# Kernel tuning notes

Hardware: AMD Instinct MI355X
Metric: run time of the kernel (lower is better)

Reference implementation:

```python
import jax, jax.numpy as jnp
import numpy as np

N_P = 50000   # number of 'place' nodes
N_A = 50000   # number of 'a_transition' nodes
E = 1600000   # edges per edge type
IN = 128      # input feature dim
OUT = 64      # HANConv out_channels
H = 4         # heads
D = OUT // H  # per-head dim
HID = 64      # decoder hidden
NEG_SLOPE = 0.2  # HANConv leaky_relu slope


def setup_inputs() -> dict:
    key = jax.random.key(0)
    ks = jax.random.split(key, 24)
    def nrm(i, shape, scale=1.0):
        return jax.random.normal(ks[i], shape, dtype=jnp.float32) * scale
    w = lambda i, shape, fan: nrm(i, shape, (1.0 / fan) ** 0.5)
    return {
        "x_place": nrm(0, (N_P, IN)),
        "x_atrans": nrm(1, (N_A, IN)),
        "e_pa_src": jax.random.randint(ks[2], (E,), 0, N_P),
        "e_pa_dst": jax.random.randint(ks[3], (E,), 0, N_A),
        "e_aa_src": jax.random.randint(ks[4], (E,), 0, N_A),
        "e_aa_dst": jax.random.randint(ks[5], (E,), 0, N_A),
        "e_ap_src": jax.random.randint(ks[6], (E,), 0, N_A),
        "e_ap_dst": jax.random.randint(ks[7], (E,), 0, N_P),
        "Wp_place": w(8, (IN, OUT), IN),
        "bp_place": jnp.zeros((OUT,), jnp.float32),
        "Wp_atrans": w(9, (IN, OUT), IN),
        "bp_atrans": jnp.zeros((OUT,), jnp.float32),
        "asrc_pa": w(10, (H, D), D),
        "adst_pa": w(11, (H, D), D),
        "asrc_aa": w(12, (H, D), D),
        "adst_aa": w(13, (H, D), D),
        "asrc_ap": w(14, (H, D), D),
        "adst_ap": w(15, (H, D), D),
        "Wk": w(16, (OUT, OUT), OUT),
        "bk": jnp.zeros((OUT,), jnp.float32),
        "q": w(17, (OUT,), OUT),
        "Wd1": w(18, (OUT, HID), OUT),
        "bd1": jnp.zeros((HID,), jnp.float32),
        "Wd2": w(19, (HID, 1), HID),
        "bd2": jnp.zeros((1,), jnp.float32),
    }


def _edge_conv(h_src, h_dst, a_src, a_dst, src, dst, n_dst):
    """HANConv node-level attention for one edge type.
    h_src: [N_src, H, D], h_dst: [N_dst, H, D]; returns relu-aggregated [n_dst, H*D]."""
    alpha = (h_src * a_src).sum(-1)[src] + (h_dst * a_dst).sum(-1)[dst]  # [E, H]
    alpha = jax.nn.leaky_relu(alpha, NEG_SLOPE)
    amax = jax.ops.segment_max(alpha, dst, num_segments=n_dst)
    amax = jnp.where(jnp.isfinite(amax), amax, 0.0)  # guard empty neighborhoods
    ex = jnp.exp(alpha - amax[dst])
    den = jax.ops.segment_sum(ex, dst, num_segments=n_dst) + 1e-16  # PyG softmax eps
    wgt = ex / den[dst]                           # scatter-softmax per dst node [E, H]
    msg = h_src[src] * wgt[:, :, None]            # [E, H, D]
    out = jax.ops.segment_sum(msg, dst, num_segments=n_dst)
    return jax.nn.relu(out.reshape(n_dst, H * D))


def _semantic(outs, q, Wk, bk):
    """HANConv semantic-level attention over edge-type embeddings."""
    stk = jnp.stack(outs)                                       # [T, N, OUT]
    score = (q * jnp.tanh(stk @ Wk + bk).mean(axis=1)).sum(-1)  # [T]
    attn = jax.nn.softmax(score)
    return jnp.einsum('t,tnc->nc', attn, stk)


def reference(x_place, x_atrans, e_pa_src, e_pa_dst, e_aa_src, e_aa_dst, e_ap_src, e_ap_dst,
              Wp_place, bp_place, Wp_atrans, bp_atrans,
              asrc_pa, adst_pa, asrc_aa, adst_aa, asrc_ap, adst_ap,
              Wk, bk, q, Wd1, bd1, Wd2, bd2):
    # per-node-type projection, split into heads
    h_p = (x_place @ Wp_place + bp_place).reshape(N_P, H, D)
    h_a = (x_atrans @ Wp_atrans + bp_atrans).reshape(N_A, H, D)
    # node-level attention per edge type
    out_pa = _edge_conv(h_p, h_a, asrc_pa, adst_pa, e_pa_src, e_pa_dst, N_A)
    out_aa = _edge_conv(h_a, h_a, asrc_aa, adst_aa, e_aa_src, e_aa_dst, N_A)
    out_ap = _edge_conv(h_a, h_p, asrc_ap, adst_ap, e_ap_src, e_ap_dst, N_P)
    # semantic-level attention per destination node type
    x_a = _semantic([out_pa, out_aa], q, Wk, bk)   # 'a_transition'
    _xp = _semantic([out_ap], q, Wk, bk)           # 'place' (computed by encoder, unused downstream)
    # decoder MLP on 'a_transition' + softmax over nodes (dim=0)
    z = jax.nn.relu(x_a @ Wd1 + bd1) @ Wd2 + bd2   # [N_A, 1]
    return jax.nn.softmax(z, axis=0)
```

## Files before the change

kernel.cpp:

```cpp
#include <hip/hip_runtime.h>
#include <hip/hip_fp16.h>
#include <math.h>

#define NP 50000
#define NA 50000
#define NE 1600000
#define IN_DIM 128
#define OUT_DIM 64

#define NB 391
#define BCAP 4608
#define P1_CHUNK 4096
#define P1_GRID ((NE + P1_CHUNK - 1) / P1_CHUNK)
#define PROJ_BLOCKS ((NP + 63) / 64)

typedef _Float16 v8h __attribute__((ext_vector_type(8)));
typedef _Float16 h2f __attribute__((ext_vector_type(2)));
typedef float    v4f __attribute__((ext_vector_type(4)));

__device__ inline float fast_tanh(float x) {
    const float e = __expf(2.f * x);
    return 1.f - 2.f / (e + 1.f);
}

__device__ inline float lane_f32(float v, int k) {
    return __builtin_bit_cast(float,
        __builtin_amdgcn_readlane(__builtin_bit_cast(int, v), k));
}

__global__ __launch_bounds__(256) void front_kernel(
    const float* __restrict__ xA, const float* __restrict__ WA, const float* __restrict__ bA,
    const float* __restrict__ xB, const float* __restrict__ WB, const float* __restrict__ bB,
    const float* __restrict__ a_pa_src, const float* __restrict__ a_pa_dst,
    const float* __restrict__ a_aa_src, const float* __restrict__ a_aa_dst,
    ushort* __restrict__ hA, ushort* __restrict__ hB,
    float* __restrict__ s_p_src_pa, float* __restrict__ s_a_dst_pa,
    float* __restrict__ s_a_src_aa, float* __restrict__ s_a_dst_aa,
    const int* __restrict__ srcA, const int* __restrict__ dstA,
    const int* __restrict__ srcB, const int* __restrict__ dstB,
    int* __restrict__ gpart, int* __restrict__ gcur)
{
    __shared__ __align__(16) char smem[22656];
    const int type = blockIdx.y;
    const int tid = threadIdx.x;

    if (blockIdx.x < P1_GRID) {
        const int* src = type ? srcB : srcA;
        const int* dst = type ? dstB : dstA;
        const int ebase = blockIdx.x * P1_CHUNK;
        const int ecount = min(P1_CHUNK, NE - ebase);

        int* hist   = (int*)smem;
        int* starts = hist + NB;
        int* offs2  = starts + NB;
        int* gbase  = offs2 + NB;
        unsigned* sorted = (unsigned*)(gbase + NB);

        for (int i = tid; i < NB; i += 256) hist[i] = 0;
        __syncthreads();
        for (int i = tid; i < ecount; i += 256)
            atomicAdd(&hist[dst[ebase + i] >> 7], 1);
        __syncthreads();
        if (tid < 64) {
            int carry = 0;
            for (int r = 0; r < 7; ++r) {
                const int idx = r * 64 + tid;
                const int v = (idx < NB) ? hist[idx] : 0;
                int s = v;
                #pragma unroll
                for (int off = 1; off < 64; off <<= 1) {
                    const int t = __shfl_up(s, off);
                    if (tid >= off) s += t;
                }
                if (idx < NB) { starts[idx] = carry + s - v; offs2[idx] = carry + s - v; }
                carry += __shfl(s, 63);
            }
        }
        __syncthreads();
        for (int i = tid; i < ecount; i += 256) {
            const int d = dst[ebase + i];
            const int s = src[ebase + i];
            const int bin = d >> 7;
            const int pos = atomicAdd(&offs2[bin], 1);
            sorted[pos] = ((unsigned)bin << 23) | ((unsigned)(d & 127) << 16) | (unsigned)s;
        }
        __syncthreads();
        for (int b = tid; b < NB; b += 256) {
            const int cnt = hist[b];
            const int flatb = type * NB + b;
            gbase[b] = cnt ? (flatb * BCAP + atomicAdd(&gcur[flatb], cnt)) : 0;
        }
        __syncthreads();
        for (int i = tid; i < ecount; i += 256) {
            const unsigned e = sorted[i];
            const int bin = e >> 23;
            gpart[gbase[bin] + (i - starts[bin])] = (int)(e & 0x7FFFFF);
        }
        return;
    }

    const int pbid = blockIdx.x - P1_GRID;
    const float* x = type ? xB : xA;
    const float* W = type ? WB : WA;
    const float* bias = type ? bB : bA;
    ushort* h_out  = type ? hB : hA;
    const float* c0 = type ? a_pa_dst : a_pa_src;
    float*       s0 = type ? s_a_dst_pa : s_p_src_pa;
    const float* c1 = type ? a_aa_src : nullptr;
    float*       s1 = type ? s_a_src_aa : nullptr;
    const float* c2 = type ? a_aa_dst : nullptr;
    float*       s2 = type ? s_a_dst_aa : nullptr;

    _Float16 (*Wt)[136] = (_Float16(*)[136])smem;
    {
        const float4* W4 = (const float4*)W;
        #pragma unroll
        for (int i = 0; i < 8; ++i) {
            const int f4i = tid + 256 * i;
            const float4 w = W4[f4i];
            const int k = f4i >> 4, c4 = (f4i & 15) * 4;
            Wt[c4 + 0][k] = (_Float16)w.x;
            Wt[c4 + 1][k] = (_Float16)w.y;
            Wt[c4 + 2][k] = (_Float16)w.z;
            Wt[c4 + 3][k] = (_Float16)w.w;
        }
    }
    __syncthreads();

    const int lane = tid & 63;
    const int wid = tid >> 6;
    const int node0 = (pbid * 4 + wid) * 16;
    if (node0 >= NP) return;
    const int m = lane & 15;
    const int quad = lane >> 4;

    v4f acc[4] = {};
    #pragma unroll
    for (int kc = 0; kc < 4; ++kc) {
        const int k0 = kc * 32 + quad * 8;
        const float4 xa = *(const float4*)(x + (size_t)(node0 + m) * IN_DIM + k0);
        const float4 xb2 = *(const float4*)(x + (size_t)(node0 + m) * IN_DIM + k0 + 4);
        v8h af;
        af[0] = (_Float16)xa.x;  af[1] = (_Float16)xa.y;
        af[2] = (_Float16)xa.z;  af[3] = (_Float16)xa.w;
        af[4] = (_Float16)xb2.x; af[5] = (_Float16)xb2.y;
        af[6] = (_Float16)xb2.z; af[7] = (_Float16)xb2.w;
        #pragma unroll
        for (int cb = 0; cb < 4; ++cb) {
            const v8h bf = *(const v8h*)&Wt[cb * 16 + m][k0];
            acc[cb] = __builtin_amdgcn_mfma_f32_16x16x32_f16(af, bf, acc[cb], 0, 0, 0);
        }
    }

    #pragma unroll
    for (int cb = 0; cb < 4; ++cb) {
        const int c = cb * 16 + m;
        const float bv = bias[c];
        float hv[4];
        #pragma unroll
        for (int r = 0; r < 4; ++r) {
            hv[r] = acc[cb][r] + bv;
            const int node = node0 + quad * 4 + r;
            h_out[(size_t)node * 64 + c] = __half_as_ushort(__float2half_rn(hv[r]));
        }
        #define DO_SCORE(A, S)                                         \
            if (A) {                                                   \
                const float av = (A)[c];                               \
                float v0 = hv[0]*av, v1 = hv[1]*av, v2 = hv[2]*av, v3 = hv[3]*av; \
                for (int msk = 1; msk <= 8; msk <<= 1) {               \
                    v0 += __shfl_xor(v0, msk);                         \
                    v1 += __shfl_xor(v1, msk);                         \
                    v2 += __shfl_xor(v2, msk);                         \
                    v3 += __shfl_xor(v3, msk);                         \
                }                                                      \
                if (m == 0) {                                          \
                    const int nb = node0 + quad * 4;                   \
                    (S)[(nb + 0) * 4 + cb] = v0;                       \
                    (S)[(nb + 1) * 4 + cb] = v1;                       \
                    (S)[(nb + 2) * 4 + cb] = v2;                       \
                    (S)[(nb + 3) * 4 + cb] = v3;                       \
                }                                                      \
            }
        DO_SCORE(c0, s0)
        DO_SCORE(c1, s1)
        DO_SCORE(c2, s2)
        #undef DO_SCORE
    }
}

__global__ __launch_bounds__(256) void bucket_sort_kernel(
    int* __restrict__ gpart, const int* __restrict__ gcur,
    int* __restrict__ recA, int* __restrict__ offsA,
    int* __restrict__ recB, int* __restrict__ offsB)
{
    const int b = blockIdx.x, type = blockIdx.y;
    int* rec  = type ? recB  : recA;
    int* offs = type ? offsB : offsA;
    const int flat = type * NB + b;
    const int region = flat * BCAP;
    const int cnt = gcur[flat];
    const int tid = threadIdx.x;

    __shared__ int hist[128];
    __shared__ int starts[128];
    __shared__ int offs2[128];
    __shared__ int red[4];
    __shared__ int sorted[BCAP];

    int p = 0;
    for (int i = tid; i < b; i += 256) p += gcur[type * NB + i];
    #pragma unroll
    for (int msk = 1; msk <= 32; msk <<= 1) p += __shfl_xor(p, msk);
    if ((tid & 63) == 0) red[tid >> 6] = p;
    if (tid < 128) hist[tid] = 0;
    __syncthreads();
    const int bst = red[0] + red[1] + red[2] + red[3];

    for (int i = tid; i < cnt; i += 256)
        atomicAdd(&hist[gpart[region + i] >> 16], 1);
    __syncthreads();
    if (tid < 64) {
        int carry = 0;
        for (int r = 0; r < 2; ++r) {
            const int idx = r * 64 + tid;
            const int v = hist[idx];
            int s = v;
            #pragma unroll
            for (int off = 1; off < 64; off <<= 1) {
                const int t = __shfl_up(s, off);
                if (tid >= off) s += t;
            }
            starts[idx] = carry + s - v;
            offs2[idx]  = carry + s - v;
            carry += __shfl(s, 63);
        }
    }
    __syncthreads();
    for (int i = tid; i < cnt; i += 256) {
        const int pk = gpart[region + i];
        const int pos = atomicAdd(&offs2[pk >> 16], 1);
        sorted[pos] = pk & 0xFFFF;
    }
    __syncthreads();
    for (int i = tid; i < cnt; i += 256) rec[bst + i] = sorted[i];
    if (tid < 128) {
        const int n = b * 128 + tid;
        if (n < NA) offs[n] = bst + starts[tid];
    }
    if (b == NB - 1 && tid == 0) offs[NA] = bst + cnt;
}

__global__ __launch_bounds__(256) void gather_kernel(
    const int* __restrict__ offsA, const int* __restrict__ recA,
    const ushort* __restrict__ hA, const float* __restrict__ ssA,
    const float* __restrict__ sdA, float* __restrict__ outA,
    const int* __restrict__ offsB, const int* __restrict__ recB,
    const ushort* __restrict__ hB, const float* __restrict__ ssB,
    const float* __restrict__ sdB, float* __restrict__ outB, int n_dst)
{
    const int type = blockIdx.y;
    const int* offs = type ? offsB : offsA;
    const int* rec  = type ? recB  : recA;
    const ushort* h_src = type ? hB : hA;
    const float* s_src = type ? ssB : ssA;
    const float* s_dst = type ? sdB : sdA;
    float* outbuf = type ? outB : outA;

    const int lane = threadIdx.x & 63;
    const int d = blockIdx.x * 4 + (threadIdx.x >> 6);
    if (d >= n_dst) return;
    const int q = lane & 7;
    const int sub = lane >> 3;
    const int h = q >> 1;
    const float sd = s_dst[d * 4 + h];
    const ushort* hq = h_src + (q << 3);
    const float* ss = s_src + h;
    const int beg = offs[d], end = offs[d + 1];

    float acc[8] = {};
    float wacc = 0.f;
    for (int base = beg; base < end; base += 64) {
        const int c64 = min(64, end - base);
        const int sv = (lane < c64) ? rec[base + lane] : 0;
        const int iters = (c64 + 7) >> 3;
        for (int it = 0; it < iters; ++it) {
            const int idx = it * 8 + sub;
            const int s = __shfl(sv, idx);
            if (idx < c64) {
                float alpha = ss[(size_t)s * 4] + sd;
                alpha = fmaxf(alpha, 0.2f * alpha);
                const float w = __expf(alpha);
                const uint4 pk = *(const uint4*)(hq + ((size_t)s << 6));
                const h2f a0 = __builtin_bit_cast(h2f, pk.x);
                const h2f a1 = __builtin_bit_cast(h2f, pk.y);
                const h2f a2 = __builtin_bit_cast(h2f, pk.z);
                const h2f a3 = __builtin_bit_cast(h2f, pk.w);
                acc[0] = fmaf((float)a0[0], w, acc[0]);
                acc[1] = fmaf((float)a0[1], w, acc[1]);
                acc[2] = fmaf((float)a1[0], w, acc[2]);
                acc[3] = fmaf((float)a1[1], w, acc[3]);
                acc[4] = fmaf((float)a2[0], w, acc[4]);
                acc[5] = fmaf((float)a2[1], w, acc[5]);
                acc[6] = fmaf((float)a3[0], w, acc[6]);
                acc[7] = fmaf((float)a3[1], w, acc[7]);
                wacc += w;
            }
        }
    }
    #pragma unroll
    for (int m = 8; m <= 32; m <<= 1) {
        #pragma unroll
        for (int j = 0; j < 8; ++j) acc[j] += __shfl_xor(acc[j], m);
        wacc += __shfl_xor(wacc, m);
    }
    if (sub == 0) {
        const float inv = 1.f / (wacc + 1e-16f);
        float4 o0, o1;
        o0.x = fmaxf(acc[0] * inv, 0.f);
        o0.y = fmaxf(acc[1] * inv, 0.f);
        o0.z = fmaxf(acc[2] * inv, 0.f);
        o0.w = fmaxf(acc[3] * inv, 0.f);
        o1.x = fmaxf(acc[4] * inv, 0.f);
        o1.y = fmaxf(acc[5] * inv, 0.f);
        o1.z = fmaxf(acc[6] * inv, 0.f);
        o1.w = fmaxf(acc[7] * inv, 0.f);
        float* op = outbuf + (size_t)d * 64 + q * 8;
        *(float4*)op = o0;
        *(float4*)(op + 4) = o1;
    }
}

#define SEM_BLOCKS 512
__global__ __launch_bounds__(256) void semantic_kernel(
    const float* __restrict__ out0, const float* __restrict__ out1,
    const float* __restrict__ Wk, const float* __restrict__ bk,
    float* __restrict__ sem, int n)
{
    const int c = threadIdx.x, ty = threadIdx.y;
    float wk[64];
    #pragma unroll
    for (int k = 0; k < 64; ++k) wk[k] = Wk[k * 64 + c];
    const float bkc = bk[c];
    float acc0 = 0.f, acc1 = 0.f;
    for (int node = blockIdx.x * 4 + ty; node < n; node += SEM_BLOCKS * 4) {
        const float n0 = out0[(size_t)node * 64 + c];
        const float n1 = out1[(size_t)node * 64 + c];
        float a0 = bkc, a1 = bkc;
        #pragma unroll
        for (int k = 0; k < 64; ++k) {
            a0 = fmaf(lane_f32(n0, k), wk[k], a0);
            a1 = fmaf(lane_f32(n1, k), wk[k], a1);
        }
        acc0 += fast_tanh(a0);
        acc1 += fast_tanh(a1);
    }
    __shared__ float red[2][4][64];
    red[0][ty][c] = acc0; red[1][ty][c] = acc1;
    __syncthreads();
    if (ty == 0) {
        atomicAdd(&sem[c],      red[0][0][c] + red[0][1][c] + red[0][2][c] + red[0][3][c]);
        atomicAdd(&sem[64 + c], red[1][0][c] + red[1][1][c] + red[1][2][c] + red[1][3][c]);
    }
}

__global__ __launch_bounds__(256) void decoder_kernel(
    const float* __restrict__ out0, const float* __restrict__ out1,
    const float* __restrict__ sem, const float* __restrict__ qv,
    const float* __restrict__ Wd1, const float* __restrict__ bd1,
    const float* __restrict__ Wd2, const float* __restrict__ bd2,
    float* __restrict__ z, int n)
{
    __shared__ float attn_s[2];
    const int c = threadIdx.x, ty = threadIdx.y;
    const int node = blockIdx.x * 4 + ty;

    if (ty == 0) {
        float v0 = sem[c] * qv[c];
        float v1 = sem[64 + c] * qv[c];
        for (int off = 32; off >= 1; off >>= 1) {
            v0 += __shfl_xor(v0, off);
            v1 += __shfl_xor(v1, off);
        }
        if (c == 0) {
            const float t0 = v0 / (float)NA, t1 = v1 / (float)NA;
            const float m = fmaxf(t0, t1);
            const float e0 = __expf(t0 - m), e1 = __expf(t1 - m);
            const float inv = 1.f / (e0 + e1);
            attn_s[0] = e0 * inv;
            attn_s[1] = e1 * inv;
        }
    }
    float wd[64];
    #pragma unroll
    for (int k = 0; k < 64; ++k) wd[k] = Wd1[k * 64 + c];
    __syncthreads();
    if (node >= n) return;
    const float a0 = attn_s[0], a1 = attn_s[1];
    const float xv = a0 * out0[(size_t)node * 64 + c]
                   + a1 * out1[(size_t)node * 64 + c];
    float acc = bd1[c];
    #pragma unroll
    for (int k = 0; k < 64; ++k)
        acc = fmaf(lane_f32(xv, k), wd[k], acc);
    float hv = fmaxf(acc, 0.f) * Wd2[c];
    for (int off = 32; off >= 1; off >>= 1) hv += __shfl_xor(hv, off);
    if (c == 0) z[node] = hv + bd2[0];
}

__global__ __launch_bounds__(256) void softmax_exp_kernel(
    const float* __restrict__ z, float* __restrict__ e,
    float* __restrict__ esum, int n)
{
    float part = 0.f;
    for (int i = blockIdx.x * 256 + threadIdx.x; i < n; i += gridDim.x * 256) {
        const float v = __expf(z[i]);
        e[i] = v;
        part += v;
    }
    for (int off = 32; off >= 1; off >>= 1) part += __shfl_xor(part, off);
    __shared__ float red[4];
    if ((threadIdx.x & 63) == 0) red[threadIdx.x >> 6] = part;
    __syncthreads();
    if (threadIdx.x == 0)
        atomicAdd(esum, red[0] + red[1] + red[2] + red[3]);
}

__global__ __launch_bounds__(256) void softmax_final_kernel(
    const float* __restrict__ e, const float* __restrict__ esum,
    float* __restrict__ out, int n)
{
    const int i = blockIdx.x * 256 + threadIdx.x;
    if (i < n) out[i] = e[i] / (*esum);
}

extern "C" void kernel_launch(void* const* d_in, const int* in_sizes, int n_in,
                              void* d_out, int out_size, void* d_ws, size_t ws_size,
                              hipStream_t stream)
{
    const float* x_place  = (const float*)d_in[0];
    const float* x_atrans = (const float*)d_in[1];
    const int* e_pa_src = (const int*)d_in[2];
    const int* e_pa_dst = (const int*)d_in[3];
    const int* e_aa_src = (const int*)d_in[4];
    const int* e_aa_dst = (const int*)d_in[5];
    const float* Wp_place  = (const float*)d_in[8];
    const float* bp_place  = (const float*)d_in[9];
    const float* Wp_atrans = (const float*)d_in[10];
    const float* bp_atrans = (const float*)d_in[11];
    const float* asrc_pa = (const float*)d_in[12];
    const float* adst_pa = (const float*)d_in[13];
    const float* asrc_aa = (const float*)d_in[14];
    const float* adst_aa = (const float*)d_in[15];
    const float* Wk  = (const float*)d_in[18];
    const float* bk  = (const float*)d_in[19];
    const float* q   = (const float*)d_in[20];
    const float* Wd1 = (const float*)d_in[21];
    const float* bd1 = (const float*)d_in[22];
    const float* Wd2 = (const float*)d_in[23];
    const float* bd2 = (const float*)d_in[24];
    float* out = (float*)d_out;

    float* ws = (float*)d_ws;
    size_t off = 0;
    auto alloc = [&](size_t n) {
        float* p = ws + off; off += (n + 3) & ~(size_t)3; return p;
    };

    ushort* h_p       = (ushort*)alloc((size_t)NP * 32);
    ushort* h_a       = (ushort*)alloc((size_t)NA * 32);
    float* s_p_src_pa = alloc((size_t)NP * 4);
    float* s_a_dst_pa = alloc((size_t)NA * 4);
    float* s_a_src_aa = alloc((size_t)NA * 4);
    float* s_a_dst_aa = alloc((size_t)NA * 4);
    float* out_pa     = alloc((size_t)NA * 64);
    float* out_aa     = alloc((size_t)NA * 64);
    int*   offs_pa    = (int*)alloc(NA + 1);
    int*   offs_aa    = (int*)alloc(NA + 1);
    int*   rec_pa     = (int*)alloc(NE);
    int*   rec_aa     = (int*)alloc(NE);
    int*   gcur       = (int*)alloc(2 * NB);
    float* sem        = alloc(128);
    float* esum       = alloc(4);
    float* zbuf       = alloc(NA);
    float* ebuf       = alloc(NA);
    int* gpart = (int*)out_pa;
    (void)ws_size; (void)in_sizes; (void)n_in; (void)out_size;

    const size_t zbytes = (size_t)((char*)(esum + 4) - (char*)gcur);
    hipMemsetAsync(gcur, 0, zbytes, stream);

    front_kernel<<<dim3(P1_GRID + PROJ_BLOCKS, 2), 256, 0, stream>>>(
        x_place, Wp_place, bp_place,
        x_atrans, Wp_atrans, bp_atrans,
        asrc_pa, adst_pa, asrc_aa, adst_aa,
        h_p, h_a,
        s_p_src_pa, s_a_dst_pa, s_a_src_aa, s_a_dst_aa,
        e_pa_src, e_pa_dst, e_aa_src, e_aa_dst, gpart, gcur);

    bucket_sort_kernel<<<dim3(NB, 2), 256, 0, stream>>>(
        gpart, gcur, rec_pa, offs_pa, rec_aa, offs_aa);

    gather_kernel<<<dim3((NA + 3) / 4, 2), 256, 0, stream>>>(
        offs_pa, rec_pa, h_p, s_p_src_pa, s_a_dst_pa, out_pa,
        offs_aa, rec_aa, h_a, s_a_src_aa, s_a_dst_aa, out_aa, NA);

    dim3 b64x4(64, 4);
    semantic_kernel<<<SEM_BLOCKS, b64x4, 0, stream>>>(out_pa, out_aa, Wk, bk, sem, NA);
    decoder_kernel<<<NA / 4, b64x4, 0, stream>>>(
        out_pa, out_aa, sem, q, Wd1, bd1, Wd2, bd2, zbuf, NA);
    softmax_exp_kernel<<<196, 256, 0, stream>>>(zbuf, ebuf, esum, NA);
    softmax_final_kernel<<<(NA + 255) / 256, 256, 0, stream>>>(ebuf, esum, out, NA);
}
```

Before: 332.4 us.

## Replace two-pass bucket sort CSR build with degree histogram and atomic scatter

Builds the CSR from per-node global atomic degree counts, a per-block prefix-sum offsets kernel, and a scatter kernel that places each edge with a per-node atomic cursor. This replaces the shared-memory bucket partition and in-bucket local sort. It adds one kernel launch and relies on random-address global atomics plus scattered writes. Edge order within each row becomes nondeterministic, so floating-point summation order can vary from run to run. The offs kernel rescans all prior degrees in every block, which is quadratic-ish redundant reading.

```diff
diff --git a/kernel.cpp b/kernel.cpp
--- a/kernel.cpp
+++ b/kernel.cpp
@@ -9,9 +9,10 @@
 #define OUT_DIM 64
 
 #define NB 391
-#define BCAP 4608
-#define P1_CHUNK 4096
-#define P1_GRID ((NE + P1_CHUNK - 1) / P1_CHUNK)
+#define HIST_CHUNK 4096
+#define HIST_GRID ((NE + HIST_CHUNK - 1) / HIST_CHUNK)
+#define SC_CHUNK 2048
+#define SC_GRID ((NE + SC_CHUNK - 1) / SC_CHUNK)
 #define PROJ_BLOCKS ((NP + 63) / 64)
 
 typedef _Float16 v8h __attribute__((ext_vector_type(8)));
@@ -36,70 +37,24 @@
     ushort* __restrict__ hA, ushort* __restrict__ hB,
     float* __restrict__ s_p_src_pa, float* __restrict__ s_a_dst_pa,
     float* __restrict__ s_a_src_aa, float* __restrict__ s_a_dst_aa,
-    const int* __restrict__ srcA, const int* __restrict__ dstA,
-    const int* __restrict__ srcB, const int* __restrict__ dstB,
-    int* __restrict__ gpart, int* __restrict__ gcur)
-{
-    __shared__ __align__(16) char smem[22656];
+    const int* __restrict__ dstA, const int* __restrict__ dstB,
+    int* __restrict__ deg)
+{
+    __shared__ _Float16 Wt[64][136];
     const int type = blockIdx.y;
     const int tid = threadIdx.x;
 
-    if (blockIdx.x < P1_GRID) {
-        const int* src = type ? srcB : srcA;
+    if (blockIdx.x < HIST_GRID) {
         const int* dst = type ? dstB : dstA;
-        const int ebase = blockIdx.x * P1_CHUNK;
-        const int ecount = min(P1_CHUNK, NE - ebase);
-
-        int* hist   = (int*)smem;
-        int* starts = hist + NB;
-        int* offs2  = starts + NB;
-        int* gbase  = offs2 + NB;
-        unsigned* sorted = (unsigned*)(gbase + NB);
-
-        for (int i = tid; i < NB; i += 256) hist[i] = 0;
-        __syncthreads();
+        int* degt = deg + type * NA;
+        const int ebase = blockIdx.x * HIST_CHUNK;
+        const int ecount = min(HIST_CHUNK, NE - ebase);
         for (int i = tid; i < ecount; i += 256)
-            atomicAdd(&hist[dst[ebase + i] >> 7], 1);
-        __syncthreads();
-        if (tid < 64) {
-            int carry = 0;
-            for (int r = 0; r < 7; ++r) {
-                const int idx = r * 64 + tid;
-                const int v = (idx < NB) ? hist[idx] : 0;
-                int s = v;
-                #pragma unroll
-                for (int off = 1; off < 64; off <<= 1) {
-                    const int t = __shfl_up(s, off);
-                    if (tid >= off) s += t;
-                }
-                if (idx < NB) { starts[idx] = carry + s - v; offs2[idx] = carry + s - v; }
-                carry += __shfl(s, 63);
-            }
-        }
-        __syncthreads();
-        for (int i = tid; i < ecount; i += 256) {
-            const int d = dst[ebase + i];
-            const int s = src[ebase + i];
-            const int bin = d >> 7;
-            const int pos = atomicAdd(&offs2[bin], 1);
-            sorted[pos] = ((unsigned)bin << 23) | ((unsigned)(d & 127) << 16) | (unsigned)s;
-        }
-        __syncthreads();
-        for (int b = tid; b < NB; b += 256) {
-            const int cnt = hist[b];
-            const int flatb = type * NB + b;
-            gbase[b] = cnt ? (flatb * BCAP + atomicAdd(&gcur[flatb], cnt)) : 0;
-        }
-        __syncthreads();
-        for (int i = tid; i < ecount; i += 256) {
-            const unsigned e = sorted[i];
-            const int bin = e >> 23;
-            gpart[gbase[bin] + (i - starts[bin])] = (int)(e & 0x7FFFFF);
-        }
+            atomicAdd(&degt[dst[ebase + i]], 1);
         return;
     }
 
-    const int pbid = blockIdx.x - P1_GRID;
+    const int pbid = blockIdx.x - HIST_GRID;
     const float* x = type ? xB : xA;
     const float* W = type ? WB : WA;
     const float* bias = type ? bB : bA;
@@ -111,7 +66,6 @@
     const float* c2 = type ? a_aa_dst : nullptr;
     float*       s2 = type ? s_a_dst_aa : nullptr;
 
-    _Float16 (*Wt)[136] = (_Float16(*)[136])smem;
     {
         const float4* W4 = (const float4*)W;
         #pragma unroll
@@ -188,66 +142,68 @@
     }
 }
 
-__global__ __launch_bounds__(256) void bucket_sort_kernel(
-    int* __restrict__ gpart, const int* __restrict__ gcur,
-    int* __restrict__ recA, int* __restrict__ offsA,
-    int* __restrict__ recB, int* __restrict__ offsB)
+__global__ __launch_bounds__(256) void offs_kernel(
+    const int* __restrict__ deg, int* __restrict__ offsA, int* __restrict__ offsB)
 {
     const int b = blockIdx.x, type = blockIdx.y;
-    int* rec  = type ? recB  : recA;
+    const int* degt = deg + type * NA;
     int* offs = type ? offsB : offsA;
-    const int flat = type * NB + b;
-    const int region = flat * BCAP;
-    const int cnt = gcur[flat];
     const int tid = threadIdx.x;
-
-    __shared__ int hist[128];
-    __shared__ int starts[128];
-    __shared__ int offs2[128];
+    const int n0 = b * 128;
+
     __shared__ int red[4];
-    __shared__ int sorted[BCAP];
+    __shared__ int dg[128], st[128];
+    __shared__ int tot;
 
     int p = 0;
-    for (int i = tid; i < b; i += 256) p += gcur[type * NB + i];
-    #pragma unroll
-    for (int msk = 1; msk <= 32; msk <<= 1) p += __shfl_xor(p, msk);
+    for (int i = tid; i < n0; i += 256) p += degt[i];
+    #pragma unroll
+    for (int m = 1; m <= 32; m <<= 1) p += __shfl_xor(p, m);
     if ((tid & 63) == 0) red[tid >> 6] = p;
-    if (tid < 128) hist[tid] = 0;
-    __syncthreads();
-    const int bst = red[0] + red[1] + red[2] + red[3];
-
-    for (int i = tid; i < cnt; i += 256)
-        atomicAdd(&hist[gpart[region + i] >> 16], 1);
-    __syncthreads();
+    if (tid < 128) dg[tid] = (n0 + tid < NA) ? degt[n0 + tid] : 0;
+    __syncthreads();
+    const int base = red[0] + red[1] + red[2] + red[3];
     if (tid < 64) {
         int carry = 0;
         for (int r = 0; r < 2; ++r) {
             const int idx = r * 64 + tid;
-            const int v = hist[idx];
+            const int v = dg[idx];
             int s = v;
             #pragma unroll
             for (int off = 1; off < 64; off <<= 1) {
                 const int t = __shfl_up(s, off);
                 if (tid >= off) s += t;
             }
-            starts[idx] = carry + s - v;
-            offs2[idx]  = carry + s - v;
+            st[idx] = carry + s - v;
             carry += __shfl(s, 63);
         }
-    }
-    __syncthreads();
-    for (int i = tid; i < cnt; i += 256) {
-        const int pk = gpart[region + i];
-        const int pos = atomicAdd(&offs2[pk >> 16], 1);
-        sorted[pos] = pk & 0xFFFF;
-    }
-    __syncthreads();
-    for (int i = tid; i < cnt; i += 256) rec[bst + i] = sorted[i];
-    if (tid < 128) {
-        const int n = b * 128 + tid;
-        if (n < NA) offs[n] = bst + starts[tid];
-    }
-    if (b == NB - 1 && tid == 0) offs[NA] = bst + cnt;
+        if (tid == 0) tot = carry;
+    }
+    __syncthreads();
+    if (tid < 128 && n0 + tid < NA) offs[n0 + tid] = base + st[tid];
+    if (b == NB - 1 && tid == 0) offs[NA] = base + tot;
+}
+
+__global__ __launch_bounds__(256) void scatter_kernel(
+    const int* __restrict__ srcA, const int* __restrict__ dstA,
+    const int* __restrict__ srcB, const int* __restrict__ dstB,
+    const int* __restrict__ offsA, const int* __restrict__ offsB,
+    int* __restrict__ cur, int* __restrict__ recA, int* __restrict__ recB)
+{
+    const int type = blockIdx.y;
+    const int* src = type ? srcB : srcA;
+    const int* dst = type ? dstB : dstA;
+    const int* offs = type ? offsB : offsA;
+    int* rec = type ? recB : recA;
+    int* curt = cur + type * NA;
+    const int ebase = blockIdx.x * SC_CHUNK;
+    const int ecount = min(SC_CHUNK, NE - ebase);
+    for (int i = threadIdx.x; i < ecount; i += 256) {
+        const int d = dst[ebase + i];
+        const int s = src[ebase + i];
+        const int pos = atomicAdd(&curt[d], 1);
+        rec[offs[d] + pos] = s;
+    }
 }
 
 __global__ __launch_bounds__(256) void gather_kernel(
@@ -478,27 +434,29 @@
     int*   offs_aa    = (int*)alloc(NA + 1);
     int*   rec_pa     = (int*)alloc(NE);
     int*   rec_aa     = (int*)alloc(NE);
-    int*   gcur       = (int*)alloc(2 * NB);
+    int*   deg        = (int*)alloc(2 * NA);
+    int*   cur        = (int*)alloc(2 * NA);
     float* sem        = alloc(128);
     float* esum       = alloc(4);
     float* zbuf       = alloc(NA);
     float* ebuf       = alloc(NA);
-    int* gpart = (int*)out_pa;
     (void)ws_size; (void)in_sizes; (void)n_in; (void)out_size;
 
-    const size_t zbytes = (size_t)((char*)(esum + 4) - (char*)gcur);
-    hipMemsetAsync(gcur, 0, zbytes, stream);
-
-    front_kernel<<<dim3(P1_GRID + PROJ_BLOCKS, 2), 256, 0, stream>>>(
+    const size_t zbytes = (size_t)((char*)(esum + 4) - (char*)deg);
+    hipMemsetAsync(deg, 0, zbytes, stream);
+
+    front_kernel<<<dim3(HIST_GRID + PROJ_BLOCKS, 2), 256, 0, stream>>>(
         x_place, Wp_place, bp_place,
         x_atrans, Wp_atrans, bp_atrans,
         asrc_pa, adst_pa, asrc_aa, adst_aa,
         h_p, h_a,
         s_p_src_pa, s_a_dst_pa, s_a_src_aa, s_a_dst_aa,
-        e_pa_src, e_pa_dst, e_aa_src, e_aa_dst, gpart, gcur);
-
-    bucket_sort_kernel<<<dim3(NB, 2), 256, 0, stream>>>(
-        gpart, gcur, rec_pa, offs_pa, rec_aa, offs_aa);
+        e_pa_dst, e_aa_dst, deg);
+
+    offs_kernel<<<dim3(NB, 2), 256, 0, stream>>>(deg, offs_pa, offs_aa);
+    scatter_kernel<<<dim3(SC_GRID, 2), 256, 0, stream>>>(
+        e_pa_src, e_pa_dst, e_aa_src, e_aa_dst,
+        offs_pa, offs_aa, cur, rec_pa, rec_aa);
 
     gather_kernel<<<dim3((NA + 3) / 4, 2), 256, 0, stream>>>(
         offs_pa, rec_pa, h_p, s_p_src_pa, s_a_dst_pa, out_pa,
```

New measurement: 598.2 us. +80.0%, slower.
